# Performance work log

Hardware: AMD Instinct MI355X
Metric: run time of the kernel (lower is better)

The kernel has to match this reference:

```python
import jax, jax.numpy as jnp
import numpy as np

BATCH, SEQ, D_IN, D_STATE = 8, 4096, 1024, 64


def setup_inputs() -> dict:
    key = jax.random.key(0)
    ks = jax.random.split(key, 3)
    u = jax.random.normal(ks[0], (BATCH, SEQ, D_IN), dtype=jnp.float32)
    log_A = jnp.zeros((D_STATE,), dtype=jnp.float32)
    B = jax.random.normal(ks[1], (D_STATE, D_IN), dtype=jnp.float32) * 0.01
    C = jax.random.normal(ks[2], (D_IN, D_STATE), dtype=jnp.float32) * 0.01
    D = jnp.ones((D_IN,), dtype=jnp.float32)
    log_delta = jnp.zeros((D_IN,), dtype=jnp.float32)
    return {"u": u, "log_A": log_A, "B": B, "C": C, "D": D, "log_delta": log_delta}


def reference(u, log_A, B, C, D, log_delta):
    batch, seq_len, input_dim = u.shape
    state_dim = log_A.shape[0]
    delta = jax.nn.softplus(log_delta)                      # [I]
    A = -jnp.exp(log_A)                                     # [N]
    A_bar = jnp.exp(delta[:, None] * A[None, :])            # [I, N]
    A_bar_state = A_bar.mean(axis=0)                        # [N]
    B_bar = B * delta[None, :]                              # [N, I]
    # Precompute input projections for all timesteps: [B, T, N]
    Bu = jnp.einsum('ni,bti->btn', B_bar, u)
    x0 = jnp.zeros((batch, state_dim), dtype=u.dtype)

    def step(x, bu_t):
        x = x * A_bar_state[None, :] + bu_t
        return x, x

    _, xs = jax.lax.scan(step, x0, jnp.swapaxes(Bu, 0, 1))  # xs: [T, B, N]
    xs = jnp.swapaxes(xs, 0, 1)                             # [B, T, N]
    y = jnp.einsum('in,btn->bti', C, xs) + D[None, None, :] * u
    return y
```

## Files before the change

### kernel.cpp

```cpp
#include <hip/hip_runtime.h>
#include <hip/hip_bf16.h>
#include <cstdint>

#define BATCH 8
#define SEQ   4096
#define DIN   1024
#define DST   64
#define CHUNK 64
#define NC    (SEQ/CHUNK)

typedef __attribute__((ext_vector_type(8))) short short8;
typedef __attribute__((ext_vector_type(4))) short short4v;
typedef __attribute__((ext_vector_type(4))) float f32x4;

__device__ __forceinline__ short f2bf(float f) {
    union { float f; unsigned u; } v; v.f = f;
    unsigned r = v.u + 0x7fffu + ((v.u >> 16) & 1u);
    return (short)(r >> 16);
}
__device__ __forceinline__ float softplus_f(float x) {
    return (x > 20.f) ? x : log1pf(expf(x));
}

__global__ void ssm_k0(const float* __restrict__ logA, const float* __restrict__ Bm,
                       const float* __restrict__ Cm, const float* __restrict__ logdelta,
                       short* __restrict__ Bb, short* __restrict__ Cb,
                       float* __restrict__ a_o, float* __restrict__ l2a_o,
                       float* __restrict__ aL_o)
{
    __shared__ float red[256];
    int blk = blockIdx.x, tid = threadIdx.x;
    if (blk < DST) {
        int n = blk;
        float An = -expf(logA[n]);
        float acc = 0.f;
        #pragma unroll
        for (int ii = 0; ii < DIN/256; ++ii) {
            int i = ii*256 + tid;
            float dlt = softplus_f(logdelta[i]);
            Bb[n*DIN + i] = f2bf(Bm[n*DIN + i] * dlt);
            acc += expf(dlt * An);
        }
        red[tid] = acc; __syncthreads();
        for (int s = 128; s > 0; s >>= 1) {
            if (tid < s) red[tid] += red[tid + s];
            __syncthreads();
        }
        if (tid == 0) {
            float a = red[0] * (1.f/DIN);
            a_o[n]   = a;
            l2a_o[n] = log2f(a);
            float p = a;
            #pragma unroll
            for (int q = 0; q < 6; ++q) p = p*p;
            aL_o[n] = p;
        }
    } else {
        int base = (blk - DST) * (DIN*DST/16);
        for (int e = tid; e < DIN*DST/16; e += 256)
            Cb[base + e] = f2bf(Cm[base + e]);
    }
}

__global__ __launch_bounds__(256) void ssm_k1(
    const float* __restrict__ u, const short* __restrict__ Bb,
    const float* __restrict__ a_i, float* __restrict__ xloc, float* __restrict__ carry)
{
    int blk = blockIdx.x;
    int b = blk >> 6, c = blk & (NC-1);
    int tid = threadIdx.x;
    int w = tid >> 6, lane = tid & 63;
    int m = lane & 15, quad = lane >> 4;

    long row = ((long)b << 12) + (c << 6) + (w << 4) + m;
    const float* up = u + row * DIN + quad * 8;

    f32x4 acc0 = {0,0,0,0}, acc1 = {0,0,0,0}, acc2 = {0,0,0,0}, acc3 = {0,0,0,0};

    #pragma unroll 4
    for (int ks = 0; ks < DIN/32; ++ks) {
        const float4* uv = (const float4*)(up + ks*32);
        float4 ua = uv[0];
        float4 ub = uv[1];
        short8 af;
        af[0]=f2bf(ua.x); af[1]=f2bf(ua.y); af[2]=f2bf(ua.z); af[3]=f2bf(ua.w);
        af[4]=f2bf(ub.x); af[5]=f2bf(ub.y); af[6]=f2bf(ub.z); af[7]=f2bf(ub.w);
        const short* bbase = Bb + ks*32 + quad*8;
        short8 b0 = *(const short8*)(bbase + ( 0 + m)*DIN);
        short8 b1 = *(const short8*)(bbase + (16 + m)*DIN);
        short8 b2 = *(const short8*)(bbase + (32 + m)*DIN);
        short8 b3 = *(const short8*)(bbase + (48 + m)*DIN);
        acc0 = __builtin_amdgcn_mfma_f32_16x16x32_bf16(af, b0, acc0, 0,0,0);
        acc1 = __builtin_amdgcn_mfma_f32_16x16x32_bf16(af, b1, acc1, 0,0,0);
        acc2 = __builtin_amdgcn_mfma_f32_16x16x32_bf16(af, b2, acc2, 0,0,0);
        acc3 = __builtin_amdgcn_mfma_f32_16x16x32_bf16(af, b3, acc3, 0,0,0);
    }

    __shared__ float bu[CHUNK][DST];
    int trow = (w << 4) + (quad << 2);
    #pragma unroll
    for (int r = 0; r < 4; ++r) {
        bu[trow + r][ 0 + m] = acc0[r];
        bu[trow + r][16 + m] = acc1[r];
        bu[trow + r][32 + m] = acc2[r];
        bu[trow + r][48 + m] = acc3[r];
    }
    __syncthreads();

    if (tid < DST) {
        int n = tid;
        float an = a_i[n];
        float x = 0.f;
        float* xp = xloc + (((long)b << 12) + (c << 6)) * DST + n;
        #pragma unroll 8
        for (int t = 0; t < CHUNK; ++t) {
            x = x * an + bu[t][n];
            xp[(long)t * DST] = x;
        }
        carry[(b * NC + c) * DST + n] = x;
    }
}

__global__ void ssm_k2(const float* __restrict__ carry, const float* __restrict__ aL,
                       float* __restrict__ Xin)
{
    int b = blockIdx.x, n = threadIdx.x;
    float x = 0.f, al = aL[n];
    for (int c = 0; c < NC; ++c) {
        Xin[(b*NC + c)*DST + n] = x;
        x = x * al + carry[(b*NC + c)*DST + n];
    }
}

__global__ __launch_bounds__(256) void ssm_k3(
    const float* __restrict__ u, const float* __restrict__ xloc,
    const float* __restrict__ Xin, const float* __restrict__ l2a,
    const short* __restrict__ Cb, const float* __restrict__ D,
    float* __restrict__ y)
{
    int tblk = blockIdx.x;
    long t0 = (long)tblk << 4;
    int b = (int)(t0 >> 12);
    int tloc0 = (int)(t0 & (SEQ-1));
    int chunk = tloc0 >> 6;
    int jbase = tloc0 & (CHUNK-1);

    __shared__ short xb[16][DST];

    int tid = threadIdx.x;
    {
        int m  = tid >> 4;
        int n0 = (tid & 15) * 4;
        long t = t0 + m;
        int j  = jbase + m;
        float4 xv = *(const float4*)(xloc + t*DST + n0);
        float4 xi = *(const float4*)(Xin + (long)(b*NC + chunk)*DST + n0);
        float4 la = *(const float4*)(l2a + n0);
        float jp = (float)(j + 1);
        short4v xs;
        xs[0] = f2bf(xv.x + exp2f(jp*la.x)*xi.x);
        xs[1] = f2bf(xv.y + exp2f(jp*la.y)*xi.y);
        xs[2] = f2bf(xv.z + exp2f(jp*la.z)*xi.z);
        xs[3] = f2bf(xv.w + exp2f(jp*la.w)*xi.w);
        *(short4v*)(&xb[m][n0]) = xs;
    }
    __syncthreads();

    int w = tid >> 6, lane = tid & 63;
    int n16 = lane & 15, quad = lane >> 4;

    short8 a0 = *(const short8*)(&xb[n16][ 0 + quad*8]);
    short8 a1 = *(const short8*)(&xb[n16][32 + quad*8]);

    #pragma unroll 4
    for (int ii = 0; ii < 16; ++ii) {
        int i0 = (ii*4 + w) * 16;
        int i  = i0 + n16;
        const short* cb = Cb + (long)i*DST + quad*8;
        short8 b0 = *(const short8*)(cb);
        short8 b1 = *(const short8*)(cb + 32);
        f32x4 acc = {0,0,0,0};
        acc = __builtin_amdgcn_mfma_f32_16x16x32_bf16(a0, b0, acc, 0,0,0);
        acc = __builtin_amdgcn_mfma_f32_16x16x32_bf16(a1, b1, acc, 0,0,0);
        float Di = D[i];
        #pragma unroll
        for (int r = 0; r < 4; ++r) {
            long t = t0 + quad*4 + r;
            long off = t*DIN + i;
            y[off] = acc[r] + Di * u[off];
        }
    }
}

extern "C" void kernel_launch(void* const* d_in, const int* in_sizes, int n_in,
                              void* d_out, int out_size, void* d_ws, size_t ws_size,
                              hipStream_t stream)
{
    const float* u        = (const float*)d_in[0];
    const float* logA     = (const float*)d_in[1];
    const float* Bm       = (const float*)d_in[2];
    const float* Cm       = (const float*)d_in[3];
    const float* D        = (const float*)d_in[4];
    const float* logdelta = (const float*)d_in[5];
    float* y = (float*)d_out;

    char* ws = (char*)d_ws;
    float* xloc  = (float*)(ws);
    float* carry = (float*)(ws + 8u*1024*1024);
    float* Xin   = (float*)(ws + 8u*1024*1024 + 128*1024);
    short* Bb    = (short*)(ws + 8u*1024*1024 + 256*1024);
    short* Cb    = (short*)(ws + 8u*1024*1024 + 384*1024);
    float* a_o   = (float*)(ws + 8u*1024*1024 + 512*1024);
    float* l2a_o = a_o + 64;
    float* aL_o  = a_o + 128;

    hipLaunchKernelGGL(ssm_k0, dim3(DST + 16), dim3(256), 0, stream,
                       logA, Bm, Cm, logdelta, Bb, Cb, a_o, l2a_o, aL_o);
    hipLaunchKernelGGL(ssm_k1, dim3(BATCH*NC), dim3(256), 0, stream,
                       u, Bb, a_o, xloc, carry);
    hipLaunchKernelGGL(ssm_k2, dim3(BATCH), dim3(DST), 0, stream,
                       carry, aL_o, Xin);
    hipLaunchKernelGGL(ssm_k3, dim3((BATCH*SEQ)/16), dim3(256), 0, stream,
                       u, xloc, Xin, l2a_o, Cb, D, y);
}
```

Before: 306.9 us.

## Split K in chunk GEMM, parallel-scan carries, vectorize output stores

```diff
diff --git a/kernel.cpp b/kernel.cpp
--- a/kernel.cpp
+++ b/kernel.cpp
@@ -62,7 +62,7 @@
     }
 }
 
-__global__ __launch_bounds__(256) void ssm_k1(
+__global__ __launch_bounds__(512, 4) void ssm_k1(
     const float* __restrict__ u, const short* __restrict__ Bb,
     const float* __restrict__ a_i, float* __restrict__ xloc, float* __restrict__ carry)
 {
@@ -70,40 +70,42 @@
     int b = blk >> 6, c = blk & (NC-1);
     int tid = threadIdx.x;
     int w = tid >> 6, lane = tid & 63;
+    int mt = w & 3, kh = w >> 2;
     int m = lane & 15, quad = lane >> 4;
 
-    long row = ((long)b << 12) + (c << 6) + (w << 4) + m;
-    const float* up = u + row * DIN + quad * 8;
+    long row = ((long)b << 12) + (c << 6) + (mt << 4) + m;
+    const float* up = u + row * DIN + (kh << 9) + quad * 8;
+    const short* bbase0 = Bb + (kh << 9) + quad * 8;
 
     f32x4 acc0 = {0,0,0,0}, acc1 = {0,0,0,0}, acc2 = {0,0,0,0}, acc3 = {0,0,0,0};
 
-    #pragma unroll 4
-    for (int ks = 0; ks < DIN/32; ++ks) {
+    #pragma unroll 2
+    for (int ks = 0; ks < 16; ++ks) {
         const float4* uv = (const float4*)(up + ks*32);
         float4 ua = uv[0];
         float4 ub = uv[1];
         short8 af;
         af[0]=f2bf(ua.x); af[1]=f2bf(ua.y); af[2]=f2bf(ua.z); af[3]=f2bf(ua.w);
         af[4]=f2bf(ub.x); af[5]=f2bf(ub.y); af[6]=f2bf(ub.z); af[7]=f2bf(ub.w);
-        const short* bbase = Bb + ks*32 + quad*8;
-        short8 b0 = *(const short8*)(bbase + ( 0 + m)*DIN);
-        short8 b1 = *(const short8*)(bbase + (16 + m)*DIN);
-        short8 b2 = *(const short8*)(bbase + (32 + m)*DIN);
-        short8 b3 = *(const short8*)(bbase + (48 + m)*DIN);
+        const short* bb = bbase0 + ks*32;
+        short8 b0 = *(const short8*)(bb + ( 0 + m)*DIN);
+        short8 b1 = *(const short8*)(bb + (16 + m)*DIN);
+        short8 b2 = *(const short8*)(bb + (32 + m)*DIN);
+        short8 b3 = *(const short8*)(bb + (48 + m)*DIN);
         acc0 = __builtin_amdgcn_mfma_f32_16x16x32_bf16(af, b0, acc0, 0,0,0);
         acc1 = __builtin_amdgcn_mfma_f32_16x16x32_bf16(af, b1, acc1, 0,0,0);
         acc2 = __builtin_amdgcn_mfma_f32_16x16x32_bf16(af, b2, acc2, 0,0,0);
         acc3 = __builtin_amdgcn_mfma_f32_16x16x32_bf16(af, b3, acc3, 0,0,0);
     }
 
-    __shared__ float bu[CHUNK][DST];
-    int trow = (w << 4) + (quad << 2);
+    __shared__ float bu[2][CHUNK][DST];
+    int trow = (mt << 4) + (quad << 2);
     #pragma unroll
     for (int r = 0; r < 4; ++r) {
-        bu[trow + r][ 0 + m] = acc0[r];
-        bu[trow + r][16 + m] = acc1[r];
-        bu[trow + r][32 + m] = acc2[r];
-        bu[trow + r][48 + m] = acc3[r];
+        bu[kh][trow + r][ 0 + m] = acc0[r];
+        bu[kh][trow + r][16 + m] = acc1[r];
+        bu[kh][trow + r][32 + m] = acc2[r];
+        bu[kh][trow + r][48 + m] = acc3[r];
     }
     __syncthreads();
 
@@ -114,22 +116,43 @@
         float* xp = xloc + (((long)b << 12) + (c << 6)) * DST + n;
         #pragma unroll 8
         for (int t = 0; t < CHUNK; ++t) {
-            x = x * an + bu[t][n];
+            x = x * an + (bu[0][t][n] + bu[1][t][n]);
             xp[(long)t * DST] = x;
         }
         carry[(b * NC + c) * DST + n] = x;
     }
 }
 
-__global__ void ssm_k2(const float* __restrict__ carry, const float* __restrict__ aL,
-                       float* __restrict__ Xin)
-{
-    int b = blockIdx.x, n = threadIdx.x;
-    float x = 0.f, al = aL[n];
-    for (int c = 0; c < NC; ++c) {
-        Xin[(b*NC + c)*DST + n] = x;
-        x = x * al + carry[(b*NC + c)*DST + n];
-    }
+__global__ __launch_bounds__(1024) void ssm_k2(
+    const float* __restrict__ carry, const float* __restrict__ aL,
+    float* __restrict__ Xin)
+{
+    __shared__ float S[NC][DST];
+    int b = blockIdx.x, tid = threadIdx.x;
+    int c = tid >> 4, n0 = (tid & 15) * 4;
+
+    float4 s = *(const float4*)(carry + (b*NC + c)*DST + n0);
+    float4 p = *(const float4*)(aL + n0);
+    *(float4*)(&S[c][n0]) = s;
+    __syncthreads();
+
+    #pragma unroll
+    for (int st = 1; st < NC; st <<= 1) {
+        float4 prev = {0,0,0,0};
+        if (c >= st) prev = *(const float4*)(&S[c - st][n0]);
+        __syncthreads();
+        s.x += p.x * prev.x;
+        s.y += p.y * prev.y;
+        s.z += p.z * prev.z;
+        s.w += p.w * prev.w;
+        *(float4*)(&S[c][n0]) = s;
+        __syncthreads();
+        p.x *= p.x; p.y *= p.y; p.z *= p.z; p.w *= p.w;
+    }
+
+    float4 xo = {0,0,0,0};
+    if (c > 0) xo = *(const float4*)(&S[c-1][n0]);
+    *(float4*)(Xin + (b*NC + c)*DST + n0) = xo;
 }
 
 __global__ __launch_bounds__(256) void ssm_k3(
@@ -167,28 +190,31 @@
     __syncthreads();
 
     int w = tid >> 6, lane = tid & 63;
-    int n16 = lane & 15, quad = lane >> 4;
-
-    short8 a0 = *(const short8*)(&xb[n16][ 0 + quad*8]);
-    short8 a1 = *(const short8*)(&xb[n16][32 + quad*8]);
+    int l15 = lane & 15, quad = lane >> 4;
+
+    short8 xf0 = *(const short8*)(&xb[l15][ 0 + quad*8]);
+    short8 xf1 = *(const short8*)(&xb[l15][32 + quad*8]);
+    long trow = t0 + l15;
 
     #pragma unroll 4
     for (int ii = 0; ii < 16; ++ii) {
         int i0 = (ii*4 + w) * 16;
-        int i  = i0 + n16;
-        const short* cb = Cb + (long)i*DST + quad*8;
-        short8 b0 = *(const short8*)(cb);
-        short8 b1 = *(const short8*)(cb + 32);
+        const short* cb = Cb + (long)(i0 + l15)*DST + quad*8;
+        short8 c0 = *(const short8*)(cb);
+        short8 c1 = *(const short8*)(cb + 32);
         f32x4 acc = {0,0,0,0};
-        acc = __builtin_amdgcn_mfma_f32_16x16x32_bf16(a0, b0, acc, 0,0,0);
-        acc = __builtin_amdgcn_mfma_f32_16x16x32_bf16(a1, b1, acc, 0,0,0);
-        float Di = D[i];
-        #pragma unroll
-        for (int r = 0; r < 4; ++r) {
-            long t = t0 + quad*4 + r;
-            long off = t*DIN + i;
-            y[off] = acc[r] + Di * u[off];
-        }
+        acc = __builtin_amdgcn_mfma_f32_16x16x32_bf16(c0, xf0, acc, 0,0,0);
+        acc = __builtin_amdgcn_mfma_f32_16x16x32_bf16(c1, xf1, acc, 0,0,0);
+        int ibase = i0 + quad*4;
+        long off = trow*DIN + ibase;
+        float4 Dv = *(const float4*)(D + ibase);
+        float4 uv = *(const float4*)(u + off);
+        float4 out;
+        out.x = acc[0] + Dv.x * uv.x;
+        out.y = acc[1] + Dv.y * uv.y;
+        out.z = acc[2] + Dv.z * uv.z;
+        out.w = acc[3] + Dv.w * uv.w;
+        *(float4*)(y + off) = out;
     }
 }
 
@@ -216,9 +242,9 @@
 
     hipLaunchKernelGGL(ssm_k0, dim3(DST + 16), dim3(256), 0, stream,
                        logA, Bm, Cm, logdelta, Bb, Cb, a_o, l2a_o, aL_o);
-    hipLaunchKernelGGL(ssm_k1, dim3(BATCH*NC), dim3(256), 0, stream,
+    hipLaunchKernelGGL(ssm_k1, dim3(BATCH*NC), dim3(512), 0, stream,
                        u, Bb, a_o, xloc, carry);
-    hipLaunchKernelGGL(ssm_k2, dim3(BATCH), dim3(DST), 0, stream,
+    hipLaunchKernelGGL(ssm_k2, dim3(BATCH), dim3(1024), 0, stream,
                        carry, aL_o, Xin);
     hipLaunchKernelGGL(ssm_k3, dim3((BATCH*SEQ)/16), dim3(256), 0, stream,
                        u, xloc, Xin, l2a_o, Cb, D, y);
```

New measurement: 314.2 us. 2.4% more time.
